# Optimization experiments

Hardware: AMD Instinct MI355X
Metric: run time of the kernel (lower is better)

The kernel has to match this reference:

```python
import jax, jax.numpy as jnp
import numpy as np

N_NODES = 5000
K_POOL = 30
BN_EPS = 1e-5


def setup_inputs() -> dict:
    key = jax.random.key(0)
    ks = jax.random.split(key, 16)
    B, N, Din, C, H, OUT, E = 32, N_NODES, 16, 64, 128, 2, 80000
    F_tot = Din + 3 * C  # concat of input + 3 conv layers = 208
    return {
        "x": jax.random.normal(ks[0], (B, N, Din), jnp.float32),
        "age": jax.random.uniform(ks[1], (B,), jnp.float32) * 100.0,
        "edge_attr": jax.random.uniform(ks[2], (E,), jnp.float32) + 0.1,
        "W0": jax.random.normal(ks[3], (Din, C), jnp.float32) * 0.1,
        "b0": jnp.zeros((C,), jnp.float32),
        "W1": jax.random.normal(ks[4], (C, C), jnp.float32) * 0.1,
        "b1": jnp.zeros((C,), jnp.float32),
        "W2": jax.random.normal(ks[5], (C, C), jnp.float32) * 0.1,
        "b2": jnp.zeros((C,), jnp.float32),
        "g0": jnp.ones((C,), jnp.float32),
        "be0": jnp.zeros((C,), jnp.float32),
        "g1": jnp.ones((C,), jnp.float32),
        "be1": jnp.zeros((C,), jnp.float32),
        "mW0": jax.random.normal(ks[6], (K_POOL * F_tot + 1, H), jnp.float32) * 0.02,
        "mb0": jnp.zeros((H,), jnp.float32),
        "mW1": jax.random.normal(ks[7], (H, OUT), jnp.float32) * 0.1,
        "mb1": jnp.zeros((OUT,), jnp.float32),
        "edge_row": jax.random.randint(ks[8], (E,), 0, N, jnp.int32),
        "edge_col": jax.random.randint(ks[9], (E,), 0, N, jnp.int32),
    }


def _spmm(xw, rows, cols, nv):
    # xw: (B, N, C); out[b, r] = sum_{edges (r,c)} nv * xw[b, c]
    def one(xb):
        return jax.ops.segment_sum(xb[cols] * nv[:, None], rows, num_segments=N_NODES)
    return jax.vmap(one)(xw)


def reference(x, age, edge_attr, W0, b0, W1, b1, W2, b2, g0, be0, g1, be1,
              mW0, mb0, mW1, mb1, edge_row, edge_col):
    N = N_NODES
    # GCN normalization on A + I (gcn_norm with edge weights, self-loop value 1)
    loop = jnp.arange(N, dtype=edge_row.dtype)
    rows = jnp.concatenate([edge_row, loop])
    cols = jnp.concatenate([edge_col, loop])
    vals = jnp.concatenate([edge_attr, jnp.ones((N,), edge_attr.dtype)])
    deg = jax.ops.segment_sum(vals, rows, num_segments=N)
    dinv = jnp.where(deg > 0, jax.lax.rsqrt(jnp.maximum(deg, 1e-12)), 0.0)
    nv = dinv[rows] * vals * dinv[cols]

    feats = [x]
    h = x
    convs = [(W0, b0), (W1, b1), (W2, b2)]
    bns = [(g0, be0), (g1, be1)]
    for i, (W, b) in enumerate(convs):
        h = _spmm(h @ W, rows, cols, nv) + b  # GCNConv
        if i < len(convs) - 1:
            g, be = bns[i]
            mu = jnp.mean(h, axis=(0, 1))   # BatchNorm1d over flattened (B*N, C)
            var = jnp.var(h, axis=(0, 1))
            h = (h - mu) * jax.lax.rsqrt(var + BN_EPS) * g + be
        h = jax.nn.relu(h)  # dropout p=0.0 -> identity
        feats.append(h)

    z = jnp.concatenate(feats, axis=-1)  # (B, N, 208)
    # global_sort_pool: sort nodes by last feature channel, descending, take top-k
    order = jnp.argsort(-z[:, :, -1], axis=1)[:, :K_POOL]  # (B, k)
    zk = jnp.take_along_axis(z, order[:, :, None], axis=1)  # (B, k, 208)
    flat = zk.reshape(z.shape[0], -1)
    flat = jnp.concatenate([flat, age[:, None]], axis=1)  # append age scalar

    hm = jax.nn.relu(flat @ mW0 + mb0)  # MLP head
    out = hm @ mW1 + mb1
    return jax.nn.log_softmax(out, axis=-1)
```

## Files before the change

kernel.cpp:

```cpp
#include <hip/hip_runtime.h>
#include <math.h>

#define NN    5000
#define NE    80000
#define NB    32
#define DIN   16
#define CH    64
#define KPOOL 30
#define FTOT  208
#define FLATW 6241
#define NH    128
#define NG    8
#define GB    4
#define NPB   16
#define NCHUNK 313
#define NPAD  5008
#define NEPAD (NE + 4 * NN)
#define NSLOT 32



__global__ void k_init(float* deg, int* counts, float* stats, float* hm, int* perm) {
    int i = blockIdx.x * 256 + threadIdx.x;
    if (i < NN) { deg[i] = 1.0f; counts[i] = 0; }
    if (i < 2 * NSLOT * 128) stats[i] = 0.0f;
    if (i < 4096) hm[i] = 0.0f;
    if (i >= NN && i < NPAD) perm[i] = NN;
}

#define NEB 313
__global__ void k_edges(const float* __restrict__ attr, const int* __restrict__ erow,
                        float* deg, int* counts) {
    int e = blockIdx.x * 256 + threadIdx.x;
    if (e < NE) {
        int r = erow[e];
        atomicAdd(&deg[r], attr[e]);
        atomicAdd(&counts[r], 1);
    }
}

__global__ __launch_bounds__(1024) void k_phase1(
        const int* __restrict__ counts, const float* __restrict__ deg,
        int* rowptr, int* cursor, float* dinv, int* perm,
        const float* __restrict__ x, float* __restrict__ xt) {
    __shared__ int wsum[16], woff[16];
    __shared__ int carry_sh;
    __shared__ int hist[256];
    int t = threadIdx.x;
    if (blockIdx.x >= 2) {
        int idx = (blockIdx.x - 2) * 1024 + t;
        if (idx >= NB * NN) return;
        int b = idx / NN, n = idx % NN;
        int g = b >> 2, bi = b & 3;
        const float4* src = (const float4*)(x + (size_t)idx * DIN);
        float4* dst = (float4*)(xt + (((size_t)g * NN + n) * GB + bi) * DIN);
        dst[0] = src[0]; dst[1] = src[1]; dst[2] = src[2]; dst[3] = src[3];
        return;
    }
    if (blockIdx.x == 0) {
        int lane = t & 63, wid = t >> 6;
        if (t == 0) carry_sh = 0;
        __syncthreads();
        for (int base = 0; base < NN; base += 1024) {
            int carry = carry_sh;
            int i = base + t;
            int v = 0;
            if (i < NN) {
                v = (counts[i] + 3) & ~3;
                dinv[i] = 1.0f / sqrtf(deg[i]);
            }
            int s = v;
#pragma unroll
            for (int off = 1; off < 64; off <<= 1) {
                int o = __shfl_up(s, off);
                if (lane >= off) s += o;
            }
            if (lane == 63) wsum[wid] = s;
            __syncthreads();
            if (t < 16) {
                int w = wsum[t];
#pragma unroll
                for (int off = 1; off < 16; off <<= 1) {
                    int o = __shfl_up(w, off);
                    if (t >= off) w += o;
                }
                woff[t] = w;
            }
            __syncthreads();
            int inc = s + (wid > 0 ? woff[wid - 1] : 0) + carry;
            if (i < NN) {
                rowptr[i + 1] = inc;
                cursor[i] = inc - v;
            }
            if (t == 1023) carry_sh = carry + woff[15];
            __syncthreads();
        }
        if (t == 0) rowptr[0] = 0;
    } else {
        if (t < 256) hist[t] = 0;
        __syncthreads();
        for (int i = t; i < NN; i += 1024) {
            int b = 255 - min(((counts[i] + 3) & ~3) >> 2, 255);
            atomicAdd(&hist[b], 1);
        }
        __syncthreads();
        int mycnt = (t < 256) ? hist[t] : 0;
        for (int off = 1; off < 256; off <<= 1) {
            int v = (t < 256 && t >= off) ? hist[t - off] : 0;
            __syncthreads();
            if (t < 256) hist[t] += v;
            __syncthreads();
        }
        if (t < 256) hist[t] -= mycnt;
        __syncthreads();
        for (int i = t; i < NN; i += 1024) {
            int b = 255 - min(((counts[i] + 3) & ~3) >> 2, 255);
            int pos = atomicAdd(&hist[b], 1);
            perm[pos] = i;
        }
    }
}

__global__ __launch_bounds__(1024) void k_build(
        const int* __restrict__ erow, const int* __restrict__ ecol,
        const float* __restrict__ attr, const float* __restrict__ dinv,
        const int* __restrict__ counts, const int* __restrict__ rowptr,
        int* cursor, int* csr_col, float* csr_nv) {
    int t = blockIdx.x * 1024 + threadIdx.x;
    if (t < NE) {
        int r = erow[t], c = ecol[t];
        int pos = atomicAdd(&cursor[r], 1);
        csr_col[pos] = c;
        csr_nv[pos] = dinv[r] * attr[t] * dinv[c];
    } else if (t - NE < NN) {
        int i = t - NE;
        int cnt = counts[i];
        int pcnt = (cnt + 3) & ~3;
        int base = rowptr[i + 1] - pcnt;
        for (int p = base + cnt; p < base + pcnt; ++p) { csr_col[p] = i; csr_nv[p] = 0.0f; }
    }
}

template<int ACT>
__device__ __forceinline__ float4 actv(float4 v, float4 s, float4 t) {
    if (ACT) {
        v.x = fmaxf(fmaf(v.x, s.x, t.x), 0.f);
        v.y = fmaxf(fmaf(v.y, s.y, t.y), 0.f);
        v.z = fmaxf(fmaf(v.z, s.z, t.z), 0.f);
        v.w = fmaxf(fmaf(v.w, s.w, t.w), 0.f);
    }
    return v;
}
__device__ __forceinline__ void fma4(float4& a, float w, float4 v) {
    a.x = fmaf(w, v.x, a.x); a.y = fmaf(w, v.y, a.y);
    a.z = fmaf(w, v.z, a.z); a.w = fmaf(w, v.w, a.w);
}

template<int CIN, int ACT, int STATS, int SCORE>
__global__ __launch_bounds__(256) void k_layer(
        const float* __restrict__ in, const float* __restrict__ bnstats,
        const float* __restrict__ gamma, const float* __restrict__ beta,
        const float* __restrict__ W, const float* __restrict__ bias,
        const int* __restrict__ rowptr, const int* __restrict__ csr_col,
        const float* __restrict__ csr_nv, const float* __restrict__ dinv,
        const int* __restrict__ perm,
        float* __restrict__ out, float* __restrict__ stats,
        float* __restrict__ score) {
    constexpr int ALS = (CIN == 64) ? 68 : 20;
    __shared__ float As[4 * 16 * ALS];
    __shared__ float stl[ACT ? 128 : 4];
    int tid = threadIdx.x;
    int wid = tid >> 6, lane = tid & 63;
    int g = blockIdx.x & 7;
    int nb = (blockIdx.x >> 3) * NPB;
    int base = nb + wid * 4;
    float* Aw = As + wid * 16 * ALS;
    const int4 pid = *(const int4*)(perm + base);

    if (ACT) {
        if (tid < 64) {
            float su = 0.f, qu = 0.f;
#pragma unroll
            for (int s = 0; s < NSLOT; ++s) {
                su += bnstats[s * 128 + tid];
                qu += bnstats[s * 128 + 64 + tid];
            }
            const float inv = 1.0f / (float)(NB * NN);
            float mu = su * inv;
            float var = qu * inv - mu * mu;
            float sc = gamma[tid] / sqrtf(var + 1e-5f);
            stl[tid] = sc;
            stl[64 + tid] = fmaf(-mu, sc, beta[tid]);
        }
        __syncthreads();
    }

    if (CIN == 64) {
        const float4* __restrict__ in4 = (const float4*)in + (size_t)g * NN * 64;
        int c4 = lane & 15, bi = lane >> 4;
        float4 sv = {1.f,1.f,1.f,1.f}, tv = {0.f,0.f,0.f,0.f};
        if (ACT) { sv = ((const float4*)stl)[c4]; tv = ((const float4*)(stl + 64))[c4]; }
#pragma unroll
        for (int pr = 0; pr < 2; ++pr) {
            int id0 = (pr == 0) ? pid.x : pid.z;
            int id1 = (pr == 0) ? pid.y : pid.w;
            bool vn0 = id0 < NN, vn1 = id1 < NN;
            int rc0 = vn0 ? id0 : 0, rc1 = vn1 ? id1 : 0;
            float dd0 = dinv[rc0]; dd0 *= dd0;
            float dd1 = dinv[rc1]; dd1 *= dd1;
            float4 a0 = {0.f,0.f,0.f,0.f}, a1 = {0.f,0.f,0.f,0.f};
            {
                float4 v0 = actv<ACT>(in4[(size_t)rc0 * 64 + lane], sv, tv);
                float4 v1 = actv<ACT>(in4[(size_t)rc1 * 64 + lane], sv, tv);
                if (vn0) { a0.x = dd0 * v0.x; a0.y = dd0 * v0.y; a0.z = dd0 * v0.z; a0.w = dd0 * v0.w; }
                if (vn1) { a1.x = dd1 * v1.x; a1.y = dd1 * v1.y; a1.z = dd1 * v1.z; a1.w = dd1 * v1.w; }
            }
            int p0a = rowptr[rc0], na = vn0 ? (rowptr[rc0 + 1] - p0a) >> 2 : 0;
            int p0b = rowptr[rc1], nbv = vn1 ? (rowptr[rc1 + 1] - p0b) >> 2 : 0;
            int mx = max(na, nbv);
            for (int bb = 0; bb < mx; ++bb) {
                int ea = min(p0a + 4 * bb, NEPAD - 4);
                int eb = min(p0b + 4 * bb, NEPAD - 4);
                bool va = bb < na, vb = bb < nbv;
                int4   ca = *(const int4*)(csr_col + ea);
                float4 wa = *(const float4*)(csr_nv + ea);
                int4   cb = *(const int4*)(csr_col + eb);
                float4 wb = *(const float4*)(csr_nv + eb);
                if (!va) { wa.x = 0.f; wa.y = 0.f; wa.z = 0.f; wa.w = 0.f;
                           ca.x = 0; ca.y = 0; ca.z = 0; ca.w = 0; }
                if (!vb) { wb.x = 0.f; wb.y = 0.f; wb.z = 0.f; wb.w = 0.f;
                           cb.x = 0; cb.y = 0; cb.z = 0; cb.w = 0; }
                float4 u0 = in4[(size_t)ca.x * 64 + lane];
                float4 u1 = in4[(size_t)ca.y * 64 + lane];
                float4 u2 = in4[(size_t)ca.z * 64 + lane];
                float4 u3 = in4[(size_t)ca.w * 64 + lane];
                float4 t0 = in4[(size_t)cb.x * 64 + lane];
                float4 t1 = in4[(size_t)cb.y * 64 + lane];
                float4 t2 = in4[(size_t)cb.z * 64 + lane];
                float4 t3 = in4[(size_t)cb.w * 64 + lane];
                fma4(a0, wa.x, actv<ACT>(u0, sv, tv));
                fma4(a0, wa.y, actv<ACT>(u1, sv, tv));
                fma4(a0, wa.z, actv<ACT>(u2, sv, tv));
                fma4(a0, wa.w, actv<ACT>(u3, sv, tv));
                fma4(a1, wb.x, actv<ACT>(t0, sv, tv));
                fma4(a1, wb.y, actv<ACT>(t1, sv, tv));
                fma4(a1, wb.z, actv<ACT>(t2, sv, tv));
                fma4(a1, wb.w, actv<ACT>(t3, sv, tv));
            }
            *(float4*)(Aw + ((pr * 2 + 0) * 4 + bi) * ALS + c4 * 4) = a0;
            *(float4*)(Aw + ((pr * 2 + 1) * 4 + bi) * ALS + c4 * 4) = a1;
        }
    } else {
        const float* __restrict__ inr = in + (size_t)g * NN * 64;
        int ids[4] = {pid.x, pid.y, pid.z, pid.w};
#pragma unroll
        for (int i = 0; i < 4; ++i) {
            int r = ids[i];
            float a = 0.f;
            if (r < NN) {
                float d = dinv[r];
                a = d * d * inr[(size_t)r * 64 + lane];
                int p0 = rowptr[r], p1 = rowptr[r + 1];
                for (int e = p0; e < p1; e += 4) {
                    int4   cc = *(const int4*)(csr_col + e);
                    float4 ww = *(const float4*)(csr_nv + e);
                    float v0 = inr[(size_t)cc.x * 64 + lane];
                    float v1 = inr[(size_t)cc.y * 64 + lane];
                    float v2 = inr[(size_t)cc.z * 64 + lane];
                    float v3 = inr[(size_t)cc.w * 64 + lane];
                    a = fmaf(ww.x, v0, a);
                    a = fmaf(ww.y, v1, a);
                    a = fmaf(ww.z, v2, a);
                    a = fmaf(ww.w, v3, a);
                }
            }
            Aw[(i * 4 + (lane >> 4)) * ALS + (lane & 15)] = a;
        }
    }

    int colq = lane & 15, rowq = lane >> 4;
    int node = (rowq == 0) ? pid.x : (rowq == 1) ? pid.y : (rowq == 2) ? pid.z : pid.w;

    if (!SCORE) {
        const float4* __restrict__ W4 = (const float4*)W;
        float4 bb = ((const float4*)bias)[colq];
        float4 o[4];
#pragma unroll
        for (int i = 0; i < 4; ++i) o[i] = bb;
#pragma unroll 8
        for (int k = 0; k < CIN; ++k) {
            float4 w4 = W4[k * 16 + colq];
#pragma unroll
            for (int i = 0; i < 4; ++i) {
                float a = Aw[(rowq * 4 + i) * ALS + k];
                fma4(o[i], a, w4);
            }
        }
        if (node < NN) {
            float4* __restrict__ op = (float4*)(out + ((size_t)g * NN + node) * 256);
#pragma unroll
            for (int i = 0; i < 4; ++i) op[i * 16 + colq] = o[i];
        }

        if (STATS) {
            float4 s4 = {0,0,0,0}, q4 = {0,0,0,0};
            if (node < NN) {
#pragma unroll
                for (int i = 0; i < 4; ++i) {
                    s4.x += o[i].x; s4.y += o[i].y; s4.z += o[i].z; s4.w += o[i].w;
                    q4.x = fmaf(o[i].x, o[i].x, q4.x); q4.y = fmaf(o[i].y, o[i].y, q4.y);
                    q4.z = fmaf(o[i].z, o[i].z, q4.z); q4.w = fmaf(o[i].w, o[i].w, q4.w);
                }
            }
            s4.x += __shfl_xor(s4.x, 16); s4.y += __shfl_xor(s4.y, 16);
            s4.z += __shfl_xor(s4.z, 16); s4.w += __shfl_xor(s4.w, 16);
            q4.x += __shfl_xor(q4.x, 16); q4.y += __shfl_xor(q4.y, 16);
            q4.z += __shfl_xor(q4.z, 16); q4.w += __shfl_xor(q4.w, 16);
            s4.x += __shfl_xor(s4.x, 32); s4.y += __shfl_xor(s4.y, 32);
            s4.z += __shfl_xor(s4.z, 32); s4.w += __shfl_xor(s4.w, 32);
            q4.x += __shfl_xor(q4.x, 32); q4.y += __shfl_xor(q4.y, 32);
            q4.w += __shfl_xor(q4.w, 32); q4.z += __shfl_xor(q4.z, 32);
            __syncthreads();
            if (lane < 16) {
                float* S = As + wid * 128;
                *(float4*)(S + lane * 8) = s4;
                *(float4*)(S + lane * 8 + 4) = q4;
            }
            __syncthreads();
            if (tid < 64) {
                int cq = tid >> 2, comp = tid & 3;
                float s = 0.f, q = 0.f;
#pragma unroll
                for (int w = 0; w < 4; ++w) {
                    s += As[w * 128 + cq * 8 + comp];
                    q += As[w * 128 + cq * 8 + 4 + comp];
                }
                float* sl = stats + (blockIdx.x & (NSLOT - 1)) * 128;
                atomicAdd(&sl[tid], s);
                atomicAdd(&sl[64 + tid], q);
            }
        }
    } else {
        if (node < NN) {
            float4* __restrict__ op = (float4*)(out + ((size_t)g * NN + node) * 256);
#pragma unroll
            for (int i = 0; i < 4; ++i)
                op[i * 16 + colq] = *(const float4*)(Aw + (rowq * 4 + i) * ALS + colq * 4);
        }
        if (lane < 16) {
            int q = lane >> 2;
            int nd = (q == 0) ? pid.x : (q == 1) ? pid.y : (q == 2) ? pid.z : pid.w;
            if (nd < NN) {
                float s = bias[63];
                const float* Ar = Aw + lane * ALS;
#pragma unroll 8
                for (int k = 0; k < 64; ++k)
                    s = fmaf(Ar[k], W[k * 64 + 63], s);
                score[((size_t)g * NN + nd) * 4 + (lane & 3)] = fmaxf(s, 0.f);
            }
        }
    }
}

__global__ __launch_bounds__(1024) void k_toppool(const float* __restrict__ sc, int* order,
        const float* __restrict__ stats,
        const float* __restrict__ g0, const float* __restrict__ be0,
        const float* __restrict__ g1, const float* __restrict__ be1,
        float* __restrict__ st) {
    __shared__ unsigned long long wbest[16];
    __shared__ unsigned long long winner;
    int tid = threadIdx.x;
    if (blockIdx.x == NB) {
        if (tid < 128) {
            int c = tid & 63, layer = tid >> 6;
            const float* sb = stats + layer * NSLOT * 128;
            float su = 0.f, qu = 0.f;
#pragma unroll
            for (int s = 0; s < NSLOT; ++s) {
                su += sb[s * 128 + c];
                qu += sb[s * 128 + 64 + c];
            }
            const float inv = 1.0f / (float)(NB * NN);
            float mu = su * inv;
            float var = qu * inv - mu * mu;
            float g = layer ? g1[c] : g0[c];
            float be = layer ? be1[c] : be0[c];
            float scv = g / sqrtf(var + 1e-5f);
            st[layer * 128 + c] = scv;
            st[layer * 128 + 64 + c] = fmaf(-mu, scv, be);
        }
        return;
    }
    int b = blockIdx.x;
    int g = b >> 2, bi = b & 3;
    int lane = tid & 63, wid = tid >> 6;
    unsigned long long key[5];
#pragma unroll
    for (int j = 0; j < 5; ++j) {
        int n = tid + j * 1024;
        unsigned long long k = 0;
        if (n < NN) {
            float v = sc[((size_t)g * NN + n) * GB + bi];
            k = ((unsigned long long)__float_as_uint(v) << 32) | (unsigned int)(NN - n);
        }
        key[j] = k;
    }
    for (int k = 0; k < KPOOL; ++k) {
        unsigned long long best = key[0];
#pragma unroll
        for (int j = 1; j < 5; ++j) best = (key[j] > best) ? key[j] : best;
#pragma unroll
        for (int off = 1; off < 64; off <<= 1) {
            unsigned long long o = __shfl_xor(best, off);
            best = (o > best) ? o : best;
        }
        if (lane == 0) wbest[wid] = best;
        __syncthreads();
        if (tid == 0) {
            unsigned long long w = wbest[0];
#pragma unroll
            for (int i = 1; i < 16; ++i) w = (wbest[i] > w) ? wbest[i] : w;
            winner = w;
            order[b * KPOOL + k] = NN - (int)(w & 0xFFFFFFFFu);
        }
        __syncthreads();
        int n = NN - (int)(winner & 0xFFFFFFFFu);
        if ((n & 1023) == tid) key[n >> 10] = 0;
    }
}

__global__ void k_gather(const float* __restrict__ xt, const float* __restrict__ h1,
                         const float* __restrict__ h2, const float* __restrict__ agg,
                         const float* __restrict__ W2, const float* __restrict__ b2,
                         const float* __restrict__ st, const float* __restrict__ age,
                         const int* __restrict__ order, float* __restrict__ flat) {
    int bk = blockIdx.x;
    int b = bk / KPOOL, k = bk % KPOOL;
    int n = order[bk];
    int g = b >> 2, bi = b & 3;
    size_t node = (size_t)g * NN + n;
    int f = threadIdx.x;
    float val = 0.f;
    if (f < DIN) {
        val = xt[(node * GB + bi) * DIN + f];
    } else if (f < DIN + CH) {
        int c = f - DIN;
        val = fmaxf(fmaf(h1[(node * GB + bi) * CH + c], st[c], st[64 + c]), 0.f);
    } else if (f < DIN + 2 * CH) {
        int c = f - DIN - CH;
        val = fmaxf(fmaf(h2[(node * GB + bi) * CH + c], st[128 + c], st[192 + c]), 0.f);
    } else if (f < FTOT) {
        int c = f - DIN - 2 * CH;
        const float* __restrict__ Ar = agg + (node * GB + bi) * CH;
        float s = b2[c];
#pragma unroll 8
        for (int kk = 0; kk < 64; ++kk)
            s = fmaf(Ar[kk], W2[kk * 64 + c], s);
        val = fmaxf(s, 0.f);
    }
    if (f < FTOT) flat[(size_t)b * FLATW + k * FTOT + f] = val;
    if (bk == 0 && f >= FTOT && f < FTOT + NB)
        flat[(size_t)(f - FTOT) * FLATW + (FLATW - 1)] = age[f - FTOT];
}

__global__ void k_head1(const float* __restrict__ flat, const float* __restrict__ mW0,
                        float* hm) {
    int tid = threadIdx.x;
    int j4 = (tid & 31) * 4;
    int b0 = (tid >> 5) * 4;
    int kbase = blockIdx.x * 64;
    float acc[4][4];
#pragma unroll
    for (int i = 0; i < 4; i++)
#pragma unroll
        for (int jj = 0; jj < 4; jj++) acc[i][jj] = 0.f;
    int kend = FLATW - kbase; if (kend > 64) kend = 64;
    for (int kk = 0; kk < kend; ++kk) {
        int k = kbase + kk;
        float4 w = *(const float4*)(mW0 + (size_t)k * NH + j4);
#pragma unroll
        for (int i = 0; i < 4; i++) {
            float fv = flat[(size_t)(b0 + i) * FLATW + k];
            acc[i][0] = fmaf(fv, w.x, acc[i][0]);
            acc[i][1] = fmaf(fv, w.y, acc[i][1]);
            acc[i][2] = fmaf(fv, w.z, acc[i][2]);
            acc[i][3] = fmaf(fv, w.w, acc[i][3]);
        }
    }
#pragma unroll
    for (int i = 0; i < 4; i++)
#pragma unroll
        for (int jj = 0; jj < 4; jj++)
            atomicAdd(&hm[(size_t)(b0 + i) * NH + j4 + jj], acc[i][jj]);
}

__global__ void k_head2(const float* __restrict__ hm, const float* __restrict__ mb0,
                        const float* __restrict__ mW1, const float* __restrict__ mb1,
                        float* __restrict__ out) {
    __shared__ float part[256];
    __shared__ float vals[64];
    int tid = threadIdx.x;
    int q = tid & 3, o = (tid >> 2) & 1, b = tid >> 3;
    float acc = 0.f;
    for (int j = q * 32; j < q * 32 + 32; ++j) {
        float hv = fmaxf(hm[b * NH + j] + mb0[j], 0.f);
        acc = fmaf(hv, mW1[j * 2 + o], acc);
    }
    part[tid] = acc;
    __syncthreads();
    if (tid < 64) {
        int b2 = tid >> 1, o2 = tid & 1;
        int base = (b2 << 3) + (o2 << 2);
        vals[tid] = part[base] + part[base + 1] + part[base + 2] + part[base + 3] + mb1[o2];
    }
    __syncthreads();
    if (tid < 64) {
        int b2 = tid >> 1;
        float v0 = vals[b2 * 2], v1 = vals[b2 * 2 + 1];
        float m = fmaxf(v0, v1);
        float lse = m + logf(expf(v0 - m) + expf(v1 - m));
        out[tid] = vals[tid] - lse;
    }
}

extern "C" void kernel_launch(void* const* d_in, const int* in_sizes, int n_in,
                              void* d_out, int out_size, void* d_ws, size_t ws_size,
                              hipStream_t stream) {
    const float* x    = (const float*)d_in[0];
    const float* age  = (const float*)d_in[1];
    const float* attr = (const float*)d_in[2];
    const float* W0   = (const float*)d_in[3];
    const float* b0   = (const float*)d_in[4];
    const float* W1   = (const float*)d_in[5];
    const float* b1   = (const float*)d_in[6];
    const float* W2   = (const float*)d_in[7];
    const float* b2   = (const float*)d_in[8];
    const float* g0   = (const float*)d_in[9];
    const float* be0  = (const float*)d_in[10];
    const float* g1   = (const float*)d_in[11];
    const float* be1  = (const float*)d_in[12];
    const float* mW0  = (const float*)d_in[13];
    const float* mb0  = (const float*)d_in[14];
    const float* mW1  = (const float*)d_in[15];
    const float* mb1  = (const float*)d_in[16];
    const int* erow   = (const int*)d_in[17];
    const int* ecol   = (const int*)d_in[18];
    float* out = (float*)d_out;

    float* ws     = (float*)d_ws;
    float* deg    = ws;
    float* dinv   = deg + 5008;
    int*   counts = (int*)(dinv + 5008);
    int*   rowptr = counts + 5008;
    int*   cursor = rowptr + 5008;
    int*   perm   = cursor + 5008;
    int*   csr_col= perm + 5008;
    float* csr_nv = (float*)(csr_col + NEPAD);
    float* stats  = csr_nv + NEPAD;
    float* st     = stats + 2 * NSLOT * 128;
    float* sc     = st + 256;
    int*   order  = (int*)(sc + NB * NN);
    float* flat   = (float*)(order + 960);
    float* hm     = flat + (size_t)NB * FLATW;
    float* xt     = hm + 4096;
    float* h1     = xt + (size_t)NB * NN * DIN;
    float* h2     = h1 + (size_t)NB * NN * CH;
    float* agg    = h2 + (size_t)NB * NN * CH;

    k_init<<<32, 256, 0, stream>>>(deg, counts, stats, hm, perm);
    k_edges<<<NEB, 256, 0, stream>>>(attr, erow, deg, counts);
    k_phase1<<<2 + (NB * NN + 1023) / 1024, 1024, 0, stream>>>(counts, deg, rowptr, cursor, dinv, perm, x, xt);
    k_build<<<(NE + NN + 1023) / 1024, 1024, 0, stream>>>(erow, ecol, attr, dinv, counts, rowptr, cursor, csr_col, csr_nv);

    const int NBLK = NCHUNK * NG;
    k_layer<16, 0, 1, 0><<<NBLK, 256, 0, stream>>>(xt, nullptr, nullptr, nullptr, W0, b0, rowptr, csr_col, csr_nv, dinv, perm, h1, stats, nullptr);
    k_layer<64, 1, 1, 0><<<NBLK, 256, 0, stream>>>(h1, stats, g0, be0, W1, b1, rowptr, csr_col, csr_nv, dinv, perm, h2, stats + NSLOT * 128, nullptr);
    k_layer<64, 1, 0, 1><<<NBLK, 256, 0, stream>>>(h2, stats + NSLOT * 128, g1, be1, W2, b2, rowptr, csr_col, csr_nv, dinv, perm, agg, nullptr, sc);

    k_toppool<<<NB + 1, 1024, 0, stream>>>(sc, order, stats, g0, be0, g1, be1, st);
    k_gather<<<NB * KPOOL, 256, 0, stream>>>(xt, h1, h2, agg, W2, b2, st, age, order, flat);
    k_head1<<<(FLATW + 63) / 64, 256, 0, stream>>>(flat, mW0, hm);
    k_head2<<<1, 256, 0, stream>>>(hm, mb0, mW1, mb1, out);
}
```

Baseline: 348.6 us.

## Split batch-group feature tensors into two halves to shrink gather working set

Each group of 4 batches is split into two 2-batch halves stored in separate arrays. The 64-channel layers now run as two launches per layer, each gathering float2 per lane instead of float4. The layer-1 kernel is specialised and writes both halves, outputs use nontemporal stores, and the gather kernel indexes the new split layout. The aim is to shrink the per-launch random-gather footprint so it fits better in cache, at the cost of walking the CSR twice and doubling launches.

```diff
diff --git a/kernel.cpp b/kernel.cpp
--- a/kernel.cpp
+++ b/kernel.cpp
@@ -141,23 +141,131 @@
     }
 }
 
-template<int ACT>
-__device__ __forceinline__ float4 actv(float4 v, float4 s, float4 t) {
-    if (ACT) {
-        v.x = fmaxf(fmaf(v.x, s.x, t.x), 0.f);
-        v.y = fmaxf(fmaf(v.y, s.y, t.y), 0.f);
-        v.z = fmaxf(fmaf(v.z, s.z, t.z), 0.f);
-        v.w = fmaxf(fmaf(v.w, s.w, t.w), 0.f);
-    }
-    return v;
-}
+typedef float f4n __attribute__((ext_vector_type(4)));
 __device__ __forceinline__ void fma4(float4& a, float w, float4 v) {
     a.x = fmaf(w, v.x, a.x); a.y = fmaf(w, v.y, a.y);
     a.z = fmaf(w, v.z, a.z); a.w = fmaf(w, v.w, a.w);
 }
-
-template<int CIN, int ACT, int STATS, int SCORE>
-__global__ __launch_bounds__(256) void k_layer(
+__device__ __forceinline__ void fma2(float2& a, float w, float2 v) {
+    a.x = fmaf(w, v.x, a.x); a.y = fmaf(w, v.y, a.y);
+}
+__device__ __forceinline__ float2 actv2(float2 v, float2 s, float2 t) {
+    v.x = fmaxf(fmaf(v.x, s.x, t.x), 0.f);
+    v.y = fmaxf(fmaf(v.y, s.y, t.y), 0.f);
+    return v;
+}
+__device__ __forceinline__ void nt4(float4* p, float4 v) {
+    f4n t; t.x = v.x; t.y = v.y; t.z = v.z; t.w = v.w;
+    __builtin_nontemporal_store(t, (f4n*)p);
+}
+
+__global__ __launch_bounds__(256) void k_l16(
+        const float* __restrict__ in,
+        const float* __restrict__ W, const float* __restrict__ bias,
+        const int* __restrict__ rowptr, const int* __restrict__ csr_col,
+        const float* __restrict__ csr_nv, const float* __restrict__ dinv,
+        const int* __restrict__ perm,
+        float* __restrict__ outA, float* __restrict__ outB,
+        float* __restrict__ stats) {
+    const int ALS = 20;
+    __shared__ float As[4 * 16 * ALS];
+    int tid = threadIdx.x;
+    int wid = tid >> 6, lane = tid & 63;
+    int g = blockIdx.x & 7;
+    int base = (blockIdx.x >> 3) * NPB + wid * 4;
+    float* Aw = As + wid * 16 * ALS;
+    const int4 pid = *(const int4*)(perm + base);
+
+    const float* __restrict__ inr = in + (size_t)g * NN * 64;
+    int ids[4] = {pid.x, pid.y, pid.z, pid.w};
+#pragma unroll
+    for (int i = 0; i < 4; ++i) {
+        int r = ids[i];
+        float a = 0.f;
+        if (r < NN) {
+            float d = dinv[r];
+            a = d * d * inr[(size_t)r * 64 + lane];
+            int p0 = rowptr[r], p1 = rowptr[r + 1];
+            for (int e = p0; e < p1; e += 4) {
+                int4   cc = *(const int4*)(csr_col + e);
+                float4 ww = *(const float4*)(csr_nv + e);
+                float v0 = inr[(size_t)cc.x * 64 + lane];
+                float v1 = inr[(size_t)cc.y * 64 + lane];
+                float v2 = inr[(size_t)cc.z * 64 + lane];
+                float v3 = inr[(size_t)cc.w * 64 + lane];
+                a = fmaf(ww.x, v0, a);
+                a = fmaf(ww.y, v1, a);
+                a = fmaf(ww.z, v2, a);
+                a = fmaf(ww.w, v3, a);
+            }
+        }
+        Aw[(i * 4 + (lane >> 4)) * ALS + (lane & 15)] = a;
+    }
+
+    int colq = lane & 15, rowq = lane >> 4;
+    int node = (rowq == 0) ? pid.x : (rowq == 1) ? pid.y : (rowq == 2) ? pid.z : pid.w;
+
+    const float4* __restrict__ W4 = (const float4*)W;
+    float4 bb = ((const float4*)bias)[colq];
+    float4 o[4];
+#pragma unroll
+    for (int i = 0; i < 4; ++i) o[i] = bb;
+#pragma unroll
+    for (int k = 0; k < 16; ++k) {
+        float4 w4 = W4[k * 16 + colq];
+#pragma unroll
+        for (int i = 0; i < 4; ++i) {
+            float a = Aw[(rowq * 4 + i) * ALS + k];
+            fma4(o[i], a, w4);
+        }
+    }
+    if (node < NN) {
+        float4* opA = (float4*)(outA + ((size_t)g * NN + node) * 128);
+        float4* opB = (float4*)(outB + ((size_t)g * NN + node) * 128);
+        opA[colq] = o[0]; opA[16 + colq] = o[1];
+        opB[colq] = o[2]; opB[16 + colq] = o[3];
+    }
+
+    float4 s4 = {0,0,0,0}, q4 = {0,0,0,0};
+    if (node < NN) {
+#pragma unroll
+        for (int i = 0; i < 4; ++i) {
+            s4.x += o[i].x; s4.y += o[i].y; s4.z += o[i].z; s4.w += o[i].w;
+            q4.x = fmaf(o[i].x, o[i].x, q4.x); q4.y = fmaf(o[i].y, o[i].y, q4.y);
+            q4.z = fmaf(o[i].z, o[i].z, q4.z); q4.w = fmaf(o[i].w, o[i].w, q4.w);
+        }
+    }
+    s4.x += __shfl_xor(s4.x, 16); s4.y += __shfl_xor(s4.y, 16);
+    s4.z += __shfl_xor(s4.z, 16); s4.w += __shfl_xor(s4.w, 16);
+    q4.x += __shfl_xor(q4.x, 16); q4.y += __shfl_xor(q4.y, 16);
+    q4.z += __shfl_xor(q4.z, 16); q4.w += __shfl_xor(q4.w, 16);
+    s4.x += __shfl_xor(s4.x, 32); s4.y += __shfl_xor(s4.y, 32);
+    s4.z += __shfl_xor(s4.z, 32); s4.w += __shfl_xor(s4.w, 32);
+    q4.x += __shfl_xor(q4.x, 32); q4.y += __shfl_xor(q4.y, 32);
+    q4.z += __shfl_xor(q4.z, 32); q4.w += __shfl_xor(q4.w, 32);
+    __syncthreads();
+    if (lane < 16) {
+        float* S = As + wid * 128;
+        *(float4*)(S + lane * 8) = s4;
+        *(float4*)(S + lane * 8 + 4) = q4;
+    }
+    __syncthreads();
+    if (tid < 64) {
+        int cq = tid >> 2, comp = tid & 3;
+        float s = 0.f, q = 0.f;
+#pragma unroll
+        for (int w = 0; w < 4; ++w) {
+            s += As[w * 128 + cq * 8 + comp];
+            q += As[w * 128 + cq * 8 + 4 + comp];
+        }
+        float* sl = stats + (blockIdx.x & (NSLOT - 1)) * 128;
+        atomicAdd(&sl[tid], s);
+        atomicAdd(&sl[64 + tid], q);
+    }
+}
+
+template<int SCORE>
+__global__ __launch_bounds__(256) void k_l64(
         const float* __restrict__ in, const float* __restrict__ bnstats,
         const float* __restrict__ gamma, const float* __restrict__ beta,
         const float* __restrict__ W, const float* __restrict__ bias,
@@ -165,117 +273,88 @@
         const float* __restrict__ csr_nv, const float* __restrict__ dinv,
         const int* __restrict__ perm,
         float* __restrict__ out, float* __restrict__ stats,
-        float* __restrict__ score) {
-    constexpr int ALS = (CIN == 64) ? 68 : 20;
-    __shared__ float As[4 * 16 * ALS];
-    __shared__ float stl[ACT ? 128 : 4];
+        float* __restrict__ score, int half) {
+    const int ALS = 68;
+    __shared__ float As[4 * 8 * ALS];
+    __shared__ float stl[128];
     int tid = threadIdx.x;
     int wid = tid >> 6, lane = tid & 63;
     int g = blockIdx.x & 7;
-    int nb = (blockIdx.x >> 3) * NPB;
-    int base = nb + wid * 4;
-    float* Aw = As + wid * 16 * ALS;
+    int base = (blockIdx.x >> 3) * NPB + wid * 4;
+    float* Aw = As + wid * 8 * ALS;
     const int4 pid = *(const int4*)(perm + base);
 
-    if (ACT) {
-        if (tid < 64) {
-            float su = 0.f, qu = 0.f;
-#pragma unroll
-            for (int s = 0; s < NSLOT; ++s) {
-                su += bnstats[s * 128 + tid];
-                qu += bnstats[s * 128 + 64 + tid];
-            }
-            const float inv = 1.0f / (float)(NB * NN);
-            float mu = su * inv;
-            float var = qu * inv - mu * mu;
-            float sc = gamma[tid] / sqrtf(var + 1e-5f);
-            stl[tid] = sc;
-            stl[64 + tid] = fmaf(-mu, sc, beta[tid]);
-        }
-        __syncthreads();
-    }
-
-    if (CIN == 64) {
-        const float4* __restrict__ in4 = (const float4*)in + (size_t)g * NN * 64;
-        int c4 = lane & 15, bi = lane >> 4;
-        float4 sv = {1.f,1.f,1.f,1.f}, tv = {0.f,0.f,0.f,0.f};
-        if (ACT) { sv = ((const float4*)stl)[c4]; tv = ((const float4*)(stl + 64))[c4]; }
-#pragma unroll
-        for (int pr = 0; pr < 2; ++pr) {
-            int id0 = (pr == 0) ? pid.x : pid.z;
-            int id1 = (pr == 0) ? pid.y : pid.w;
-            bool vn0 = id0 < NN, vn1 = id1 < NN;
-            int rc0 = vn0 ? id0 : 0, rc1 = vn1 ? id1 : 0;
-            float dd0 = dinv[rc0]; dd0 *= dd0;
-            float dd1 = dinv[rc1]; dd1 *= dd1;
-            float4 a0 = {0.f,0.f,0.f,0.f}, a1 = {0.f,0.f,0.f,0.f};
-            {
-                float4 v0 = actv<ACT>(in4[(size_t)rc0 * 64 + lane], sv, tv);
-                float4 v1 = actv<ACT>(in4[(size_t)rc1 * 64 + lane], sv, tv);
-                if (vn0) { a0.x = dd0 * v0.x; a0.y = dd0 * v0.y; a0.z = dd0 * v0.z; a0.w = dd0 * v0.w; }
-                if (vn1) { a1.x = dd1 * v1.x; a1.y = dd1 * v1.y; a1.z = dd1 * v1.z; a1.w = dd1 * v1.w; }
-            }
-            int p0a = rowptr[rc0], na = vn0 ? (rowptr[rc0 + 1] - p0a) >> 2 : 0;
-            int p0b = rowptr[rc1], nbv = vn1 ? (rowptr[rc1 + 1] - p0b) >> 2 : 0;
-            int mx = max(na, nbv);
-            for (int bb = 0; bb < mx; ++bb) {
-                int ea = min(p0a + 4 * bb, NEPAD - 4);
-                int eb = min(p0b + 4 * bb, NEPAD - 4);
-                bool va = bb < na, vb = bb < nbv;
-                int4   ca = *(const int4*)(csr_col + ea);
-                float4 wa = *(const float4*)(csr_nv + ea);
-                int4   cb = *(const int4*)(csr_col + eb);
-                float4 wb = *(const float4*)(csr_nv + eb);
-                if (!va) { wa.x = 0.f; wa.y = 0.f; wa.z = 0.f; wa.w = 0.f;
-                           ca.x = 0; ca.y = 0; ca.z = 0; ca.w = 0; }
-                if (!vb) { wb.x = 0.f; wb.y = 0.f; wb.z = 0.f; wb.w = 0.f;
-                           cb.x = 0; cb.y = 0; cb.z = 0; cb.w = 0; }
-                float4 u0 = in4[(size_t)ca.x * 64 + lane];
-                float4 u1 = in4[(size_t)ca.y * 64 + lane];
-                float4 u2 = in4[(size_t)ca.z * 64 + lane];
-                float4 u3 = in4[(size_t)ca.w * 64 + lane];
-                float4 t0 = in4[(size_t)cb.x * 64 + lane];
-                float4 t1 = in4[(size_t)cb.y * 64 + lane];
-                float4 t2 = in4[(size_t)cb.z * 64 + lane];
-                float4 t3 = in4[(size_t)cb.w * 64 + lane];
-                fma4(a0, wa.x, actv<ACT>(u0, sv, tv));
-                fma4(a0, wa.y, actv<ACT>(u1, sv, tv));
-                fma4(a0, wa.z, actv<ACT>(u2, sv, tv));
-                fma4(a0, wa.w, actv<ACT>(u3, sv, tv));
-                fma4(a1, wb.x, actv<ACT>(t0, sv, tv));
-                fma4(a1, wb.y, actv<ACT>(t1, sv, tv));
-                fma4(a1, wb.z, actv<ACT>(t2, sv, tv));
-                fma4(a1, wb.w, actv<ACT>(t3, sv, tv));
-            }
-            *(float4*)(Aw + ((pr * 2 + 0) * 4 + bi) * ALS + c4 * 4) = a0;
-            *(float4*)(Aw + ((pr * 2 + 1) * 4 + bi) * ALS + c4 * 4) = a1;
-        }
-    } else {
-        const float* __restrict__ inr = in + (size_t)g * NN * 64;
-        int ids[4] = {pid.x, pid.y, pid.z, pid.w};
-#pragma unroll
-        for (int i = 0; i < 4; ++i) {
-            int r = ids[i];
-            float a = 0.f;
-            if (r < NN) {
-                float d = dinv[r];
-                a = d * d * inr[(size_t)r * 64 + lane];
-                int p0 = rowptr[r], p1 = rowptr[r + 1];
-                for (int e = p0; e < p1; e += 4) {
-                    int4   cc = *(const int4*)(csr_col + e);
-                    float4 ww = *(const float4*)(csr_nv + e);
-                    float v0 = inr[(size_t)cc.x * 64 + lane];
-                    float v1 = inr[(size_t)cc.y * 64 + lane];
-                    float v2 = inr[(size_t)cc.z * 64 + lane];
-                    float v3 = inr[(size_t)cc.w * 64 + lane];
-                    a = fmaf(ww.x, v0, a);
-                    a = fmaf(ww.y, v1, a);
-                    a = fmaf(ww.z, v2, a);
-                    a = fmaf(ww.w, v3, a);
-                }
-            }
-            Aw[(i * 4 + (lane >> 4)) * ALS + (lane & 15)] = a;
-        }
+    if (tid < 64) {
+        float su = 0.f, qu = 0.f;
+#pragma unroll
+        for (int s = 0; s < NSLOT; ++s) {
+            su += bnstats[s * 128 + tid];
+            qu += bnstats[s * 128 + 64 + tid];
+        }
+        const float inv = 1.0f / (float)(NB * NN);
+        float mu = su * inv;
+        float var = qu * inv - mu * mu;
+        float sc = gamma[tid] / sqrtf(var + 1e-5f);
+        stl[tid] = sc;
+        stl[64 + tid] = fmaf(-mu, sc, beta[tid]);
+    }
+    __syncthreads();
+
+    const float2* __restrict__ in2 = (const float2*)in + (size_t)g * NN * 64;
+    float2 sv = ((const float2*)stl)[lane & 31];
+    float2 tv = ((const float2*)(stl + 64))[lane & 31];
+    int c2w = (lane & 31) << 1;
+    int biw = lane >> 5;
+
+#pragma unroll
+    for (int pr = 0; pr < 2; ++pr) {
+        int id0 = (pr == 0) ? pid.x : pid.z;
+        int id1 = (pr == 0) ? pid.y : pid.w;
+        bool vn0 = id0 < NN, vn1 = id1 < NN;
+        int rc0 = vn0 ? id0 : 0, rc1 = vn1 ? id1 : 0;
+        float dd0 = dinv[rc0]; dd0 *= dd0;
+        float dd1 = dinv[rc1]; dd1 *= dd1;
+        float2 a0 = {0.f, 0.f}, a1 = {0.f, 0.f};
+        {
+            float2 v0 = actv2(in2[(size_t)rc0 * 64 + lane], sv, tv);
+            float2 v1 = actv2(in2[(size_t)rc1 * 64 + lane], sv, tv);
+            if (vn0) { a0.x = dd0 * v0.x; a0.y = dd0 * v0.y; }
+            if (vn1) { a1.x = dd1 * v1.x; a1.y = dd1 * v1.y; }
+        }
+        int p0a = rowptr[rc0], na = vn0 ? (rowptr[rc0 + 1] - p0a) >> 2 : 0;
+        int p0b = rowptr[rc1], nbv = vn1 ? (rowptr[rc1 + 1] - p0b) >> 2 : 0;
+        int mx = max(na, nbv);
+        for (int bb = 0; bb < mx; ++bb) {
+            int ea = min(p0a + 4 * bb, NEPAD - 4);
+            int eb = min(p0b + 4 * bb, NEPAD - 4);
+            bool va = bb < na, vb = bb < nbv;
+            int4   ca = *(const int4*)(csr_col + ea);
+            float4 wa = *(const float4*)(csr_nv + ea);
+            int4   cb = *(const int4*)(csr_col + eb);
+            float4 wb = *(const float4*)(csr_nv + eb);
+            if (!va) { wa.x = 0.f; wa.y = 0.f; wa.z = 0.f; wa.w = 0.f;
+                       ca.x = 0; ca.y = 0; ca.z = 0; ca.w = 0; }
+            if (!vb) { wb.x = 0.f; wb.y = 0.f; wb.z = 0.f; wb.w = 0.f;
+                       cb.x = 0; cb.y = 0; cb.z = 0; cb.w = 0; }
+            float2 u0 = in2[(size_t)ca.x * 64 + lane];
+            float2 u1 = in2[(size_t)ca.y * 64 + lane];
+            float2 u2 = in2[(size_t)ca.z * 64 + lane];
+            float2 u3 = in2[(size_t)ca.w * 64 + lane];
+            float2 t0 = in2[(size_t)cb.x * 64 + lane];
+            float2 t1 = in2[(size_t)cb.y * 64 + lane];
+            float2 t2 = in2[(size_t)cb.z * 64 + lane];
+            float2 t3 = in2[(size_t)cb.w * 64 + lane];
+            fma2(a0, wa.x, actv2(u0, sv, tv));
+            fma2(a0, wa.y, actv2(u1, sv, tv));
+            fma2(a0, wa.z, actv2(u2, sv, tv));
+            fma2(a0, wa.w, actv2(u3, sv, tv));
+            fma2(a1, wb.x, actv2(t0, sv, tv));
+            fma2(a1, wb.y, actv2(t1, sv, tv));
+            fma2(a1, wb.z, actv2(t2, sv, tv));
+            fma2(a1, wb.w, actv2(t3, sv, tv));
+        }
+        *(float2*)(Aw + (4 * pr + biw) * ALS + c2w) = a0;
+        *(float2*)(Aw + (4 * pr + 2 + biw) * ALS + c2w) = a1;
     }
 
     int colq = lane & 15, rowq = lane >> 4;
@@ -284,71 +363,60 @@
     if (!SCORE) {
         const float4* __restrict__ W4 = (const float4*)W;
         float4 bb = ((const float4*)bias)[colq];
-        float4 o[4];
-#pragma unroll
-        for (int i = 0; i < 4; ++i) o[i] = bb;
+        float4 o0 = bb, o1 = bb;
 #pragma unroll 8
-        for (int k = 0; k < CIN; ++k) {
+        for (int k = 0; k < 64; ++k) {
             float4 w4 = W4[k * 16 + colq];
-#pragma unroll
-            for (int i = 0; i < 4; ++i) {
-                float a = Aw[(rowq * 4 + i) * ALS + k];
-                fma4(o[i], a, w4);
-            }
+            fma4(o0, Aw[(rowq * 2 + 0) * ALS + k], w4);
+            fma4(o1, Aw[(rowq * 2 + 1) * ALS + k], w4);
         }
         if (node < NN) {
-            float4* __restrict__ op = (float4*)(out + ((size_t)g * NN + node) * 256);
-#pragma unroll
-            for (int i = 0; i < 4; ++i) op[i * 16 + colq] = o[i];
-        }
-
-        if (STATS) {
-            float4 s4 = {0,0,0,0}, q4 = {0,0,0,0};
-            if (node < NN) {
-#pragma unroll
-                for (int i = 0; i < 4; ++i) {
-                    s4.x += o[i].x; s4.y += o[i].y; s4.z += o[i].z; s4.w += o[i].w;
-                    q4.x = fmaf(o[i].x, o[i].x, q4.x); q4.y = fmaf(o[i].y, o[i].y, q4.y);
-                    q4.z = fmaf(o[i].z, o[i].z, q4.z); q4.w = fmaf(o[i].w, o[i].w, q4.w);
-                }
-            }
-            s4.x += __shfl_xor(s4.x, 16); s4.y += __shfl_xor(s4.y, 16);
-            s4.z += __shfl_xor(s4.z, 16); s4.w += __shfl_xor(s4.w, 16);
-            q4.x += __shfl_xor(q4.x, 16); q4.y += __shfl_xor(q4.y, 16);
-            q4.z += __shfl_xor(q4.z, 16); q4.w += __shfl_xor(q4.w, 16);
-            s4.x += __shfl_xor(s4.x, 32); s4.y += __shfl_xor(s4.y, 32);
-            s4.z += __shfl_xor(s4.z, 32); s4.w += __shfl_xor(s4.w, 32);
-            q4.x += __shfl_xor(q4.x, 32); q4.y += __shfl_xor(q4.y, 32);
-            q4.w += __shfl_xor(q4.w, 32); q4.z += __shfl_xor(q4.z, 32);
-            __syncthreads();
-            if (lane < 16) {
-                float* S = As + wid * 128;
-                *(float4*)(S + lane * 8) = s4;
-                *(float4*)(S + lane * 8 + 4) = q4;
-            }
-            __syncthreads();
-            if (tid < 64) {
-                int cq = tid >> 2, comp = tid & 3;
-                float s = 0.f, q = 0.f;
-#pragma unroll
-                for (int w = 0; w < 4; ++w) {
-                    s += As[w * 128 + cq * 8 + comp];
-                    q += As[w * 128 + cq * 8 + 4 + comp];
-                }
-                float* sl = stats + (blockIdx.x & (NSLOT - 1)) * 128;
-                atomicAdd(&sl[tid], s);
-                atomicAdd(&sl[64 + tid], q);
-            }
+            float4* __restrict__ op = (float4*)(out + ((size_t)g * NN + node) * 128);
+            nt4(&op[colq], o0);
+            nt4(&op[16 + colq], o1);
+        }
+
+        float4 s4 = {0,0,0,0}, q4 = {0,0,0,0};
+        if (node < NN) {
+            s4.x = o0.x + o1.x; s4.y = o0.y + o1.y; s4.z = o0.z + o1.z; s4.w = o0.w + o1.w;
+            q4.x = fmaf(o0.x, o0.x, o1.x * o1.x); q4.y = fmaf(o0.y, o0.y, o1.y * o1.y);
+            q4.z = fmaf(o0.z, o0.z, o1.z * o1.z); q4.w = fmaf(o0.w, o0.w, o1.w * o1.w);
+        }
+        s4.x += __shfl_xor(s4.x, 16); s4.y += __shfl_xor(s4.y, 16);
+        s4.z += __shfl_xor(s4.z, 16); s4.w += __shfl_xor(s4.w, 16);
+        q4.x += __shfl_xor(q4.x, 16); q4.y += __shfl_xor(q4.y, 16);
+        q4.z += __shfl_xor(q4.z, 16); q4.w += __shfl_xor(q4.w, 16);
+        s4.x += __shfl_xor(s4.x, 32); s4.y += __shfl_xor(s4.y, 32);
+        s4.z += __shfl_xor(s4.z, 32); s4.w += __shfl_xor(s4.w, 32);
+        q4.x += __shfl_xor(q4.x, 32); q4.y += __shfl_xor(q4.y, 32);
+        q4.z += __shfl_xor(q4.z, 32); q4.w += __shfl_xor(q4.w, 32);
+        __syncthreads();
+        if (lane < 16) {
+            float* S = As + wid * 128;
+            *(float4*)(S + lane * 8) = s4;
+            *(float4*)(S + lane * 8 + 4) = q4;
+        }
+        __syncthreads();
+        if (tid < 64) {
+            int cq = tid >> 2, comp = tid & 3;
+            float s = 0.f, q = 0.f;
+#pragma unroll
+            for (int w = 0; w < 4; ++w) {
+                s += As[w * 128 + cq * 8 + comp];
+                q += As[w * 128 + cq * 8 + 4 + comp];
+            }
+            float* sl = stats + (blockIdx.x & (NSLOT - 1)) * 128;
+            atomicAdd(&sl[tid], s);
+            atomicAdd(&sl[64 + tid], q);
         }
     } else {
         if (node < NN) {
-            float4* __restrict__ op = (float4*)(out + ((size_t)g * NN + node) * 256);
-#pragma unroll
-            for (int i = 0; i < 4; ++i)
-                op[i * 16 + colq] = *(const float4*)(Aw + (rowq * 4 + i) * ALS + colq * 4);
-        }
-        if (lane < 16) {
-            int q = lane >> 2;
+            float4* __restrict__ op = (float4*)(out + ((size_t)g * NN + node) * 128);
+            nt4(&op[colq],      *(const float4*)(Aw + (rowq * 2 + 0) * ALS + colq * 4));
+            nt4(&op[16 + colq], *(const float4*)(Aw + (rowq * 2 + 1) * ALS + colq * 4));
+        }
+        if (lane < 8) {
+            int q = lane >> 1;
             int nd = (q == 0) ? pid.x : (q == 1) ? pid.y : (q == 2) ? pid.z : pid.w;
             if (nd < NN) {
                 float s = bias[63];
@@ -356,7 +424,7 @@
 #pragma unroll 8
                 for (int k = 0; k < 64; ++k)
                     s = fmaf(Ar[k], W[k * 64 + 63], s);
-                score[((size_t)g * NN + nd) * 4 + (lane & 3)] = fmaxf(s, 0.f);
+                score[((size_t)g * NN + nd) * 4 + half * 2 + (lane & 1)] = fmaxf(s, 0.f);
             }
         }
     }
@@ -429,8 +497,10 @@
     }
 }
 
-__global__ void k_gather(const float* __restrict__ xt, const float* __restrict__ h1,
-                         const float* __restrict__ h2, const float* __restrict__ agg,
+__global__ void k_gather(const float* __restrict__ xt,
+                         const float* __restrict__ h1a, const float* __restrict__ h1b,
+                         const float* __restrict__ h2a, const float* __restrict__ h2b,
+                         const float* __restrict__ aggA, const float* __restrict__ aggB,
                          const float* __restrict__ W2, const float* __restrict__ b2,
                          const float* __restrict__ st, const float* __restrict__ age,
                          const int* __restrict__ order, float* __restrict__ flat) {
@@ -438,20 +508,22 @@
     int b = bk / KPOOL, k = bk % KPOOL;
     int n = order[bk];
     int g = b >> 2, bi = b & 3;
-    size_t node = (size_t)g * NN + n;
+    size_t hoff = ((size_t)g * NN + n) * 2 + (bi & 1);
     int f = threadIdx.x;
     float val = 0.f;
     if (f < DIN) {
-        val = xt[(node * GB + bi) * DIN + f];
+        val = xt[(((size_t)g * NN + n) * GB + bi) * DIN + f];
     } else if (f < DIN + CH) {
         int c = f - DIN;
-        val = fmaxf(fmaf(h1[(node * GB + bi) * CH + c], st[c], st[64 + c]), 0.f);
+        const float* h = (bi < 2) ? h1a : h1b;
+        val = fmaxf(fmaf(h[hoff * 64 + c], st[c], st[64 + c]), 0.f);
     } else if (f < DIN + 2 * CH) {
         int c = f - DIN - CH;
-        val = fmaxf(fmaf(h2[(node * GB + bi) * CH + c], st[128 + c], st[192 + c]), 0.f);
+        const float* h = (bi < 2) ? h2a : h2b;
+        val = fmaxf(fmaf(h[hoff * 64 + c], st[128 + c], st[192 + c]), 0.f);
     } else if (f < FTOT) {
         int c = f - DIN - 2 * CH;
-        const float* __restrict__ Ar = agg + (node * GB + bi) * CH;
+        const float* __restrict__ Ar = ((bi < 2) ? aggA : aggB) + hoff * 64;
         float s = b2[c];
 #pragma unroll 8
         for (int kk = 0; kk < 64; ++kk)
@@ -563,9 +635,13 @@
     float* flat   = (float*)(order + 960);
     float* hm     = flat + (size_t)NB * FLATW;
     float* xt     = hm + 4096;
-    float* h1     = xt + (size_t)NB * NN * DIN;
-    float* h2     = h1 + (size_t)NB * NN * CH;
-    float* agg    = h2 + (size_t)NB * NN * CH;
+    const size_t HT = (size_t)NG * NN * 2 * CH;
+    float* h1a    = xt + (size_t)NB * NN * DIN;
+    float* h1b    = h1a + HT;
+    float* h2a    = h1b + HT;
+    float* h2b    = h2a + HT;
+    float* aggA   = h2b + HT;
+    float* aggB   = aggA + HT;
 
     k_init<<<32, 256, 0, stream>>>(deg, counts, stats, hm, perm);
     k_edges<<<NEB, 256, 0, stream>>>(attr, erow, deg, counts);
@@ -573,12 +649,14 @@
     k_build<<<(NE + NN + 1023) / 1024, 1024, 0, stream>>>(erow, ecol, attr, dinv, counts, rowptr, cursor, csr_col, csr_nv);
 
     const int NBLK = NCHUNK * NG;
-    k_layer<16, 0, 1, 0><<<NBLK, 256, 0, stream>>>(xt, nullptr, nullptr, nullptr, W0, b0, rowptr, csr_col, csr_nv, dinv, perm, h1, stats, nullptr);
-    k_layer<64, 1, 1, 0><<<NBLK, 256, 0, stream>>>(h1, stats, g0, be0, W1, b1, rowptr, csr_col, csr_nv, dinv, perm, h2, stats + NSLOT * 128, nullptr);
-    k_layer<64, 1, 0, 1><<<NBLK, 256, 0, stream>>>(h2, stats + NSLOT * 128, g1, be1, W2, b2, rowptr, csr_col, csr_nv, dinv, perm, agg, nullptr, sc);
+    k_l16<<<NBLK, 256, 0, stream>>>(xt, W0, b0, rowptr, csr_col, csr_nv, dinv, perm, h1a, h1b, stats);
+    k_l64<0><<<NBLK, 256, 0, stream>>>(h1a, stats, g0, be0, W1, b1, rowptr, csr_col, csr_nv, dinv, perm, h2a, stats + NSLOT * 128, nullptr, 0);
+    k_l64<0><<<NBLK, 256, 0, stream>>>(h1b, stats, g0, be0, W1, b1, rowptr, csr_col, csr_nv, dinv, perm, h2b, stats + NSLOT * 128, nullptr, 1);
+    k_l64<1><<<NBLK, 256, 0, stream>>>(h2a, stats + NSLOT * 128, g1, be1, W2, b2, rowptr, csr_col, csr_nv, dinv, perm, aggA, nullptr, sc, 0);
+    k_l64<1><<<NBLK, 256, 0, stream>>>(h2b, stats + NSLOT * 128, g1, be1, W2, b2, rowptr, csr_col, csr_nv, dinv, perm, aggB, nullptr, sc, 1);
 
     k_toppool<<<NB + 1, 1024, 0, stream>>>(sc, order, stats, g0, be0, g1, be1, st);
-    k_gather<<<NB * KPOOL, 256, 0, stream>>>(xt, h1, h2, agg, W2, b2, st, age, order, flat);
+    k_gather<<<NB * KPOOL, 256, 0, stream>>>(xt, h1a, h1b, h2a, h2b, aggA, aggB, W2, b2, st, age, order, flat);
     k_head1<<<(FLATW + 63) / 64, 256, 0, stream>>>(flat, mW0, hm);
     k_head2<<<1, 256, 0, stream>>>(hm, mb0, mW1, mb1, out);
 }
```

After: 423.8 us. +21.6%, slower.
